# Performance work log

Measured on AMD Instinct MI355X. Metric: run time of the kernel, lower is better.

The kernel has to match this reference:

```python
import jax, jax.numpy as jnp
import numpy as np

B, T, C, H = 4, 2048, 1024, 16
HS = C // H  # head size 64
LN_EPS = 1e-5


def setup_inputs() -> dict:
    key = jax.random.key(0)
    ks = jax.random.split(key, 14)
    s = lambda fan_in: 1.0 / np.sqrt(fan_in)
    return {
        "x": jax.random.normal(ks[0], (B, T, C), jnp.float32),
        # weights stored [in, out] (transposed vs torch nn.Linear) for y = x @ W + b
        "c_attn_w": jax.random.normal(ks[1], (C, 3 * C), jnp.float32) * s(C),
        "c_attn_b": jnp.zeros((3 * C,), jnp.float32),
        "c_proj_w": jax.random.normal(ks[2], (C, C), jnp.float32) * s(C),
        "c_proj_b": jnp.zeros((C,), jnp.float32),
        "fc_w": jax.random.normal(ks[3], (C, 4 * C), jnp.float32) * s(C),
        "fc_b": jnp.zeros((4 * C,), jnp.float32),
        "proj_w": jax.random.normal(ks[4], (4 * C, C), jnp.float32) * s(4 * C),
        "proj_b": jnp.zeros((C,), jnp.float32),
        "ln1_g": jnp.ones((C,), jnp.float32),
        "ln1_b": jnp.zeros((C,), jnp.float32),
        "ln2_g": jnp.ones((C,), jnp.float32),
        "ln2_b": jnp.zeros((C,), jnp.float32),
    }


def layer_norm(x, g, b):
    mu = jnp.mean(x, axis=-1, keepdims=True)
    var = jnp.var(x, axis=-1, keepdims=True)
    return (x - mu) * jax.lax.rsqrt(var + LN_EPS) * g + b


def attention(x, c_attn_w, c_attn_b, c_proj_w, c_proj_b):
    Bs, Ts, Cs = x.shape
    qkv = x @ c_attn_w + c_attn_b  # (B,T,3C)
    q, k, v = jnp.split(qkv, 3, axis=-1)
    q = q.reshape(Bs, Ts, H, HS).transpose(0, 2, 1, 3)  # (B,H,T,hs)
    k = k.reshape(Bs, Ts, H, HS).transpose(0, 2, 1, 3)
    v = v.reshape(Bs, Ts, H, HS).transpose(0, 2, 1, 3)
    wei = jnp.einsum("bhqd,bhkd->bhqk", q, k) * (1.0 / np.sqrt(HS))
    causal = jnp.tril(jnp.ones((Ts, Ts), bool))
    wei = jnp.where(causal, wei, -jnp.inf)
    wei = jax.nn.softmax(wei, axis=-1)
    out = jnp.einsum("bhqk,bhkd->bhqd", wei, v)
    out = out.transpose(0, 2, 1, 3).reshape(Bs, Ts, Cs)
    return out @ c_proj_w + c_proj_b


def mlp(x, fc_w, fc_b, proj_w, proj_b):
    h = jax.nn.gelu(x @ fc_w + fc_b, approximate=True)
    return h @ proj_w + proj_b


def reference(x, c_attn_w, c_attn_b, c_proj_w, c_proj_b, fc_w, fc_b, proj_w, proj_b, ln1_g, ln1_b, ln2_g, ln2_b):
    x = x + attention(layer_norm(x, ln1_g, ln1_b), c_attn_w, c_attn_b, c_proj_w, c_proj_b)
    out = x + mlp(layer_norm(x, ln2_g, ln2_b), fc_w, fc_b, proj_w, proj_b)
    return out
```

## Files before the change

### kernel.cpp

```cpp
#include <hip/hip_runtime.h>

typedef unsigned short u16;
typedef __attribute__((ext_vector_type(8))) short bf16x8;
typedef __attribute__((ext_vector_type(4))) float f32x4;

#define SC_LOG2E 0.18033688011112043f
#define MB_LOG2E 17.31234049066756f

__device__ __forceinline__ float b2f(u16 u) {
  union { unsigned int i; float f; } v; v.i = ((unsigned int)u) << 16; return v.f;
}
__device__ __forceinline__ u16 f2b(float f) {
  unsigned int x = __float_as_uint(f);
  unsigned int r = (x + 0x7fffu + ((x >> 16) & 1u)) >> 16;
  return (u16)r;
}

#define GLOAD_LDS16(g, l)                                                              \
  __builtin_amdgcn_global_load_lds((const __attribute__((address_space(1))) void*)(g), \
                                   (__attribute__((address_space(3))) void*)(l), 16, 0, 0)

__global__ __launch_bounds__(256) void transpose_cast_kernel(const float* __restrict__ in,
                                                             u16* __restrict__ out,
                                                             int K, int N) {
  __shared__ float tile[64][65];
  const int tid = threadIdx.x;
  const int n0 = blockIdx.x * 64, k0 = blockIdx.y * 64;
#pragma unroll
  for (int it = 0; it < 4; ++it) {
    int lin = it * 256 + tid;
    int r = lin >> 4, c4 = (lin & 15) * 4;
    float4 v = *(const float4*)&in[(size_t)(k0 + r) * N + n0 + c4];
    tile[r][c4 + 0] = v.x; tile[r][c4 + 1] = v.y;
    tile[r][c4 + 2] = v.z; tile[r][c4 + 3] = v.w;
  }
  __syncthreads();
#pragma unroll
  for (int it = 0; it < 2; ++it) {
    int lin = it * 256 + tid;
    int r = lin >> 3, c8 = (lin & 7) * 8;
    u16 tmp[8];
#pragma unroll
    for (int j = 0; j < 8; ++j) tmp[j] = f2b(tile[c8 + j][r]);
    *(uint4*)&out[(size_t)(n0 + r) * K + k0 + c8] = *(const uint4*)tmp;
  }
}

template <bool INF32>
__global__ __launch_bounds__(256) void ln_kernel(const void* __restrict__ xv,
                                                 const float* __restrict__ g,
                                                 const float* __restrict__ b,
                                                 u16* __restrict__ o, int C) {
  const int row = blockIdx.x, tid = threadIdx.x;
  const int wave = tid >> 6, lane = tid & 63;
  const int base = tid * 4;
  float f[4];
  if (INF32) {
    float4 v = *(const float4*)((const float*)xv + (size_t)row * C + base);
    f[0] = v.x; f[1] = v.y; f[2] = v.z; f[3] = v.w;
  } else {
    ushort4 v = *(const ushort4*)((const u16*)xv + (size_t)row * C + base);
    f[0] = b2f(v.x); f[1] = b2f(v.y); f[2] = b2f(v.z); f[3] = b2f(v.w);
  }
  float s = f[0] + f[1] + f[2] + f[3];
  float q = f[0] * f[0] + f[1] * f[1] + f[2] * f[2] + f[3] * f[3];
#pragma unroll
  for (int off = 1; off < 64; off <<= 1) {
    s += __shfl_xor(s, off);
    q += __shfl_xor(q, off);
  }
  __shared__ float reds[4], redq[4];
  if (lane == 0) { reds[wave] = s; redq[wave] = q; }
  __syncthreads();
  float S = reds[0] + reds[1] + reds[2] + reds[3];
  float Q = redq[0] + redq[1] + redq[2] + redq[3];
  const float inv = 1.0f / (float)C;
  float mean = S * inv;
  float var = Q * inv - mean * mean;
  float rs = rsqrtf(var + 1e-5f);
  float4 gv = *(const float4*)&g[base];
  float4 bv = *(const float4*)&b[base];
  ushort4 ov;
  ov.x = f2b((f[0] - mean) * rs * gv.x + bv.x);
  ov.y = f2b((f[1] - mean) * rs * gv.y + bv.y);
  ov.z = f2b((f[2] - mean) * rs * gv.z + bv.z);
  ov.w = f2b((f[3] - mean) * rs * gv.w + bv.w);
  *(ushort4*)&o[(size_t)row * C + base] = ov;
}

__device__ __forceinline__ float gelu_fn(float v) {
  float a = 0.7978845608028654f * __builtin_fmaf(0.044715f * v * v, v, v);
  float t = __builtin_amdgcn_exp2f(a * -2.8853900817779268f);
  return v * __builtin_amdgcn_rcpf(1.0f + t);
}

template <bool GELU, int RESMODE, bool OUTF32, bool VSPLIT>
__global__ __launch_bounds__(256) void gemm_kernel(const u16* __restrict__ A,
                                                   const u16* __restrict__ Bt,
                                                   const float* __restrict__ bias,
                                                   const void* __restrict__ res,
                                                   void* __restrict__ Cv,
                                                   u16* __restrict__ vt,
                                                   int M, int N, int K) {
  __shared__ u16 As[128 * 64];
  __shared__ u16 Bs[128 * 64];
  const int tid = threadIdx.x;
  const int wave = tid >> 6, lane = tid & 63;
  const int lhi = lane >> 4, llo = lane & 15;
  const int sw = llo & 7;
  const int m0 = blockIdx.x * 128, n0 = blockIdx.y * 128;
  const int wr = (wave >> 1) * 64, wc = (wave & 1) * 64;

  f32x4 acc[4][4] = {};

  for (int k0 = 0; k0 < K; k0 += 64) {
#pragma unroll
    for (int p = 0; p < 4; ++p) {
      int s = p * 256 + tid;
      int r = s >> 3;
      int c = ((s & 7) ^ (r & 7)) * 8;
      GLOAD_LDS16(A + (size_t)(m0 + r) * K + k0 + c, As + s * 8);
      GLOAD_LDS16(Bt + (size_t)(n0 + r) * K + k0 + c, Bs + s * 8);
    }
    __syncthreads();
#pragma unroll
    for (int kk = 0; kk < 2; ++kk) {
      const int cp = ((kk * 4 + lhi) ^ sw) * 8;
      bf16x8 af[4], bf[4];
#pragma unroll
      for (int i = 0; i < 4; ++i)
        af[i] = *(const bf16x8*)&As[(wr + i * 16 + llo) * 64 + cp];
#pragma unroll
      for (int j = 0; j < 4; ++j)
        bf[j] = *(const bf16x8*)&Bs[(wc + j * 16 + llo) * 64 + cp];
#pragma unroll
      for (int i = 0; i < 4; ++i)
#pragma unroll
        for (int j = 0; j < 4; ++j)
          acc[i][j] = __builtin_amdgcn_mfma_f32_16x16x32_bf16(af[i], bf[j], acc[i][j], 0, 0, 0);
    }
    __syncthreads();
  }

  const bool vblock = VSPLIT && (n0 >= 2048);
#pragma unroll
  for (int i = 0; i < 4; ++i) {
    int row = m0 + wr + i * 16 + lhi * 4;
#pragma unroll
    for (int j = 0; j < 4; ++j) {
      int col = n0 + wc + j * 16 + llo;
      float bv = bias[col];
      if (vblock) {
        const int hcol = col - 2048;
        const int bh = (row >> 11) * 16 + (hcol >> 6);
        const int d = hcol & 63;
        const int t = row & 2047;
        ushort4 tv;
        tv.x = f2b(acc[i][j][0] + bv);
        tv.y = f2b(acc[i][j][1] + bv);
        tv.z = f2b(acc[i][j][2] + bv);
        tv.w = f2b(acc[i][j][3] + bv);
        *(ushort4*)&vt[((size_t)bh * 64 + d) * 2048 + t] = tv;
        continue;
      }
#pragma unroll
      for (int r = 0; r < 4; ++r) {
        float v = acc[i][j][r] + bv;
        if (GELU) v = gelu_fn(v);
        size_t idx = (size_t)(row + r) * N + col;
        if (RESMODE == 1) v += b2f(((const u16*)res)[idx]);
        if (RESMODE == 2) v += ((const float*)res)[idx];
        if (OUTF32) ((float*)Cv)[idx] = v;
        else ((u16*)Cv)[idx] = f2b(v);
      }
    }
  }
}

__global__ __launch_bounds__(512, 4) void attn_kernel(const u16* __restrict__ qkv,
                                                      const u16* __restrict__ vt,
                                                      u16* __restrict__ out) {
  __shared__ u16 Ks[64 * 68];
  __shared__ u16 Vs[64 * 68];
  __shared__ u16 Ps[128 * 68];
  const int tid = threadIdx.x;
  const int wave = tid >> 6, lane = tid & 63;
  const int lhi = lane >> 4, llo = lane & 15;
  const int pr = blockIdx.x;
  const int bh = blockIdx.y;
  const int b = bh >> 4, h = bh & 15;
  const size_t rowbase = (size_t)b * 2048;
  const int qoff = h * 64, koff = 1024 + h * 64;
  const u16* vtb = vt + (size_t)bh * 64 * 2048;
  const int sr = tid >> 3;
  const int sc = (tid & 7) * 8;

#pragma unroll
  for (int ph = 0; ph < 2; ++ph) {
    const int qtile = ph ? pr : (15 - pr);
    const int q0 = qtile * 128;
    const int qrow = q0 + wave * 16;

    bf16x8 qf[2];
#pragma unroll
    for (int kk = 0; kk < 2; ++kk) {
      uint4 v = *(const uint4*)&qkv[(rowbase + qrow + llo) * 3072 + qoff + kk * 32 + lhi * 8];
      qf[kk] = *(const bf16x8*)&v;
    }

    f32x4 oacc[4] = {};
    float l_st[4] = {};
    const int nkt = 2 * qtile + 2;

    uint4 pk = *(const uint4*)&qkv[(rowbase + sr) * 3072 + koff + sc];
    uint4 pv = *(const uint4*)&vtb[(size_t)sr * 2048 + sc];

    for (int kt = 0; kt < nkt; ++kt) {
      const int kt0 = kt * 64;
      __syncthreads();
      *(uint4*)&Ks[sr * 68 + sc] = pk;
      *(uint4*)&Vs[sr * 68 + sc] = pv;
      __syncthreads();
      if (kt + 1 < nkt) {
        const int nt0 = kt0 + 64;
        pk = *(const uint4*)&qkv[(rowbase + nt0 + sr) * 3072 + koff + sc];
        pv = *(const uint4*)&vtb[(size_t)sr * 2048 + nt0 + sc];
      }

      if (kt0 > qrow + 15) continue;

      f32x4 s[4] = {};
#pragma unroll
      for (int kk = 0; kk < 2; ++kk)
#pragma unroll
        for (int j = 0; j < 4; ++j) {
          bf16x8 kf = *(const bf16x8*)&Ks[(j * 16 + llo) * 68 + kk * 32 + lhi * 8];
          s[j] = __builtin_amdgcn_mfma_f32_16x16x32_bf16(qf[kk], kf, s[j], 0, 0, 0);
        }

      const bool msk = (kt0 + 63 > qrow);
      u16* psrow = &Ps[(wave * 16) * 68];
#pragma unroll
      for (int j = 0; j < 4; ++j) {
        const int key = kt0 + j * 16 + llo;
#pragma unroll
        for (int r = 0; r < 4; ++r) {
          float sv = s[j][r];
          if (msk) sv = (key <= qrow + lhi * 4 + r) ? sv : -1e30f;
          float p = __builtin_amdgcn_exp2f(__builtin_fmaf(sv, SC_LOG2E, -MB_LOG2E));
          l_st[r] += p;
          psrow[(lhi * 4 + r) * 68 + j * 16 + llo] = (u16)(__float_as_uint(p) >> 16);
        }
      }

#pragma unroll
      for (int kc = 0; kc < 2; ++kc) {
        bf16x8 pf = *(const bf16x8*)&Ps[(wave * 16 + llo) * 68 + kc * 32 + lhi * 8];
#pragma unroll
        for (int j4 = 0; j4 < 4; ++j4) {
          bf16x8 vf = *(const bf16x8*)&Vs[(j4 * 16 + llo) * 68 + kc * 32 + lhi * 8];
          oacc[j4] = __builtin_amdgcn_mfma_f32_16x16x32_bf16(pf, vf, oacc[j4], 0, 0, 0);
        }
      }
    }

#pragma unroll
    for (int r = 0; r < 4; ++r) {
      float v = l_st[r];
      v += __shfl_xor(v, 1);
      v += __shfl_xor(v, 2);
      v += __shfl_xor(v, 4);
      v += __shfl_xor(v, 8);
      l_st[r] = 1.0f / v;
    }
#pragma unroll
    for (int j4 = 0; j4 < 4; ++j4)
#pragma unroll
      for (int r = 0; r < 4; ++r) {
        size_t row = rowbase + qrow + lhi * 4 + r;
        out[row * 1024 + h * 64 + j4 * 16 + llo] = f2b(oacc[j4][r] * l_st[r]);
      }
  }
}

extern "C" void kernel_launch(void* const* d_in, const int* in_sizes, int n_in,
                              void* d_out, int out_size, void* d_ws, size_t ws_size,
                              hipStream_t stream) {
  const float* x        = (const float*)d_in[0];
  const float* c_attn_w = (const float*)d_in[1];
  const float* c_attn_b = (const float*)d_in[2];
  const float* c_proj_w = (const float*)d_in[3];
  const float* c_proj_b = (const float*)d_in[4];
  const float* fc_w     = (const float*)d_in[5];
  const float* fc_b     = (const float*)d_in[6];
  const float* proj_w   = (const float*)d_in[7];
  const float* proj_b   = (const float*)d_in[8];
  const float* ln1_g    = (const float*)d_in[9];
  const float* ln1_b    = (const float*)d_in[10];
  const float* ln2_g    = (const float*)d_in[11];
  const float* ln2_b    = (const float*)d_in[12];
  float* out = (float*)d_out;
  u16* ws = (u16*)d_ws;

  const size_t M = 8192;
  u16* ln_buf = ws;
  u16* qkv    = ln_buf + M * 1024;
  u16* x1     = qkv + M * 3072;
  u16* hbuf   = x1 + M * 1024;
  u16* wT_a   = hbuf + M * 4096;
  u16* wT_p   = wT_a + 3072 * 1024;
  u16* wT_f   = wT_p + 1024 * 1024;
  u16* wT_m   = wT_f + 4096 * 1024;
  u16* vt     = hbuf;

  dim3 blk(256);
  transpose_cast_kernel<<<dim3(48, 16), blk, 0, stream>>>(c_attn_w, wT_a, 1024, 3072);
  transpose_cast_kernel<<<dim3(16, 16), blk, 0, stream>>>(c_proj_w, wT_p, 1024, 1024);
  transpose_cast_kernel<<<dim3(64, 16), blk, 0, stream>>>(fc_w, wT_f, 1024, 4096);
  transpose_cast_kernel<<<dim3(16, 64), blk, 0, stream>>>(proj_w, wT_m, 4096, 1024);

  ln_kernel<true><<<8192, blk, 0, stream>>>(x, ln1_g, ln1_b, ln_buf, 1024);
  gemm_kernel<false, 0, false, true><<<dim3(64, 24), blk, 0, stream>>>(ln_buf, wT_a, c_attn_b, nullptr, qkv, vt, 8192, 3072, 1024);
  attn_kernel<<<dim3(8, 64), dim3(512), 0, stream>>>(qkv, vt, ln_buf);
  gemm_kernel<false, 2, false, false><<<dim3(64, 8), blk, 0, stream>>>(ln_buf, wT_p, c_proj_b, x, x1, nullptr, 8192, 1024, 1024);
  ln_kernel<false><<<8192, blk, 0, stream>>>(x1, ln2_g, ln2_b, ln_buf, 1024);
  gemm_kernel<true, 0, false, false><<<dim3(64, 32), blk, 0, stream>>>(ln_buf, wT_f, fc_b, nullptr, hbuf, nullptr, 8192, 4096, 1024);
  gemm_kernel<false, 1, true, false><<<dim3(64, 8), blk, 0, stream>>>(hbuf, wT_m, proj_b, x1, out, nullptr, 8192, 1024, 4096);
}
```

Before: 477.0 us.

## Rework attention kernel to 32x32 MFMA with register-resident P and split-K waves

The attention kernel moves from 16x16x32 MFMA tiles to 32x32x16 tiles and computes S transposed (K times Q), so each lane holds the probabilities for one query row. P is packed to bf16 in registers with v_cvt_pk_bf16_f32 and exchanged across half-waves with shuffles, which removes the LDS round trip through the Ps buffer. The eight waves are now split into four row groups and two key halves, and the partial outputs and row sums are merged through LDS at the end of each phase. This costs an extra reduction, two more barriers per phase, and more LDS for Of, and the P conversion now truncates differently than before.

New measurement: 484.5 us. Within noise of the previous version (+1.6%).

```diff
diff --git a/kernel.cpp b/kernel.cpp
--- a/kernel.cpp
+++ b/kernel.cpp
@@ -3,6 +3,7 @@
 typedef unsigned short u16;
 typedef __attribute__((ext_vector_type(8))) short bf16x8;
 typedef __attribute__((ext_vector_type(4))) float f32x4;
+typedef __attribute__((ext_vector_type(16))) float f32x16;
 
 #define SC_LOG2E 0.18033688011112043f
 #define MB_LOG2E 17.31234049066756f
@@ -14,6 +15,11 @@
   unsigned int x = __float_as_uint(f);
   unsigned int r = (x + 0x7fffu + ((x >> 16) & 1u)) >> 16;
   return (u16)r;
+}
+__device__ __forceinline__ unsigned int cvtpk(float lo, float hi) {
+  unsigned int r;
+  asm volatile("v_cvt_pk_bf16_f32 %0, %1, %2" : "=v"(r) : "v"(lo), "v"(hi));
+  return r;
 }
 
 #define GLOAD_LDS16(g, l)                                                              \
@@ -182,15 +188,17 @@
                                                       u16* __restrict__ out) {
   __shared__ u16 Ks[64 * 68];
   __shared__ u16 Vs[64 * 68];
-  __shared__ u16 Ps[128 * 68];
+  __shared__ float Of[4][32][65];
+  __shared__ float Lf[4][32];
   const int tid = threadIdx.x;
   const int wave = tid >> 6, lane = tid & 63;
-  const int lhi = lane >> 4, llo = lane & 15;
+  const int l31 = lane & 31, h = lane >> 5;
+  const int rg = wave & 3, kg = wave >> 2;
   const int pr = blockIdx.x;
   const int bh = blockIdx.y;
-  const int b = bh >> 4, h = bh & 15;
+  const int b = bh >> 4, hh = bh & 15;
   const size_t rowbase = (size_t)b * 2048;
-  const int qoff = h * 64, koff = 1024 + h * 64;
+  const int qoff = hh * 64, koff = 1024 + hh * 64;
   const u16* vtb = vt + (size_t)bh * 64 * 2048;
   const int sr = tid >> 3;
   const int sc = (tid & 7) * 8;
@@ -199,17 +207,18 @@
   for (int ph = 0; ph < 2; ++ph) {
     const int qtile = ph ? pr : (15 - pr);
     const int q0 = qtile * 128;
-    const int qrow = q0 + wave * 16;
-
-    bf16x8 qf[2];
-#pragma unroll
-    for (int kk = 0; kk < 2; ++kk) {
-      uint4 v = *(const uint4*)&qkv[(rowbase + qrow + llo) * 3072 + qoff + kk * 32 + lhi * 8];
-      qf[kk] = *(const bf16x8*)&v;
-    }
-
-    f32x4 oacc[4] = {};
-    float l_st[4] = {};
+    const int qrow0 = q0 + rg * 32;
+    const int qrow = qrow0 + l31;
+
+    bf16x8 qf[4];
+#pragma unroll
+    for (int s4 = 0; s4 < 4; ++s4) {
+      uint4 v = *(const uint4*)&qkv[(rowbase + qrow) * 3072 + qoff + s4 * 16 + h * 8];
+      qf[s4] = *(const bf16x8*)&v;
+    }
+
+    f32x16 oacc[2] = {};
+    float lsum = 0.0f;
     const int nkt = 2 * qtile + 2;
 
     uint4 pk = *(const uint4*)&qkv[(rowbase + sr) * 3072 + koff + sc];
@@ -227,59 +236,74 @@
         pv = *(const uint4*)&vtb[(size_t)sr * 2048 + nt0 + sc];
       }
 
-      if (kt0 > qrow + 15) continue;
-
-      f32x4 s[4] = {};
-#pragma unroll
-      for (int kk = 0; kk < 2; ++kk)
-#pragma unroll
-        for (int j = 0; j < 4; ++j) {
-          bf16x8 kf = *(const bf16x8*)&Ks[(j * 16 + llo) * 68 + kk * 32 + lhi * 8];
-          s[j] = __builtin_amdgcn_mfma_f32_16x16x32_bf16(qf[kk], kf, s[j], 0, 0, 0);
+      const int kbase = kt0 + kg * 32;
+      if (kbase > qrow0 + 31) continue;
+
+      f32x16 s = {};
+#pragma unroll
+      for (int s4 = 0; s4 < 4; ++s4) {
+        bf16x8 kf = *(const bf16x8*)&Ks[(kg * 32 + l31) * 68 + s4 * 16 + h * 8];
+        s = __builtin_amdgcn_mfma_f32_32x32x16_bf16(kf, qf[s4], s, 0, 0, 0);
+      }
+
+      const bool msk = (kbase + 31 > qrow0);
+      float pex[16];
+#pragma unroll
+      for (int m = 0; m < 16; ++m) {
+        const int key = kbase + (m & 3) + 8 * (m >> 2) + 4 * h;
+        float sv = s[m];
+        if (msk) sv = (key <= qrow) ? sv : -1e30f;
+        float p = __builtin_amdgcn_exp2f(__builtin_fmaf(sv, SC_LOG2E, -MB_LOG2E));
+        pex[m] = p;
+        lsum += p;
+      }
+      unsigned int pw[8], xw[8];
+#pragma unroll
+      for (int rb = 0; rb < 4; ++rb)
+#pragma unroll
+        for (int p = 0; p < 2; ++p)
+          pw[rb * 2 + p] = cvtpk(pex[4 * rb + 2 * p], pex[4 * rb + 2 * p + 1]);
+#pragma unroll
+      for (int i = 0; i < 8; ++i) xw[i] = __shfl_xor((int)pw[i], 32);
+
+#pragma unroll
+      for (int sb = 0; sb < 2; ++sb) {
+        unsigned int fw[4];
+        fw[0] = h ? xw[(2 * sb + 1) * 2 + 0] : pw[(2 * sb) * 2 + 0];
+        fw[1] = h ? xw[(2 * sb + 1) * 2 + 1] : pw[(2 * sb) * 2 + 1];
+        fw[2] = h ? pw[(2 * sb + 1) * 2 + 0] : xw[(2 * sb) * 2 + 0];
+        fw[3] = h ? pw[(2 * sb + 1) * 2 + 1] : xw[(2 * sb) * 2 + 1];
+        bf16x8 pb = *(const bf16x8*)fw;
+#pragma unroll
+        for (int dg = 0; dg < 2; ++dg) {
+          bf16x8 va = *(const bf16x8*)&Vs[(dg * 32 + l31) * 68 + kg * 32 + sb * 16 + h * 8];
+          oacc[dg] = __builtin_amdgcn_mfma_f32_32x32x16_bf16(va, pb, oacc[dg], 0, 0, 0);
         }
-
-      const bool msk = (kt0 + 63 > qrow);
-      u16* psrow = &Ps[(wave * 16) * 68];
-#pragma unroll
-      for (int j = 0; j < 4; ++j) {
-        const int key = kt0 + j * 16 + llo;
-#pragma unroll
-        for (int r = 0; r < 4; ++r) {
-          float sv = s[j][r];
-          if (msk) sv = (key <= qrow + lhi * 4 + r) ? sv : -1e30f;
-          float p = __builtin_amdgcn_exp2f(__builtin_fmaf(sv, SC_LOG2E, -MB_LOG2E));
-          l_st[r] += p;
-          psrow[(lhi * 4 + r) * 68 + j * 16 + llo] = (u16)(__float_as_uint(p) >> 16);
+      }
+    }
+
+    float lkg = lsum + __shfl_xor(lsum, 32);
+    if (kg == 1) {
+#pragma unroll
+      for (int dg = 0; dg < 2; ++dg)
+#pragma unroll
+        for (int m = 0; m < 16; ++m)
+          Of[rg][l31][dg * 32 + (m & 3) + 8 * (m >> 2) + 4 * h] = oacc[dg][m];
+      if (h == 0) Lf[rg][l31] = lkg;
+    }
+    __syncthreads();
+    if (kg == 0) {
+      const float inv = 1.0f / (lkg + Lf[rg][l31]);
+#pragma unroll
+      for (int dg = 0; dg < 2; ++dg)
+#pragma unroll
+        for (int m = 0; m < 16; ++m) {
+          const int dim = dg * 32 + (m & 3) + 8 * (m >> 2) + 4 * h;
+          float o = oacc[dg][m] + Of[rg][l31][dim];
+          out[(rowbase + qrow) * 1024 + hh * 64 + dim] = f2b(o * inv);
         }
-      }
-
-#pragma unroll
-      for (int kc = 0; kc < 2; ++kc) {
-        bf16x8 pf = *(const bf16x8*)&Ps[(wave * 16 + llo) * 68 + kc * 32 + lhi * 8];
-#pragma unroll
-        for (int j4 = 0; j4 < 4; ++j4) {
-          bf16x8 vf = *(const bf16x8*)&Vs[(j4 * 16 + llo) * 68 + kc * 32 + lhi * 8];
-          oacc[j4] = __builtin_amdgcn_mfma_f32_16x16x32_bf16(pf, vf, oacc[j4], 0, 0, 0);
-        }
-      }
-    }
-
-#pragma unroll
-    for (int r = 0; r < 4; ++r) {
-      float v = l_st[r];
-      v += __shfl_xor(v, 1);
-      v += __shfl_xor(v, 2);
-      v += __shfl_xor(v, 4);
-      v += __shfl_xor(v, 8);
-      l_st[r] = 1.0f / v;
-    }
-#pragma unroll
-    for (int j4 = 0; j4 < 4; ++j4)
-#pragma unroll
-      for (int r = 0; r < 4; ++r) {
-        size_t row = rowbase + qrow + lhi * 4 + r;
-        out[row * 1024 + h * 64 + j4 * 16 + llo] = f2b(oacc[j4][r] * l_st[r]);
-      }
+    }
+    __syncthreads();
   }
 }
 
```
